# Performance work log

Measured on AMD Instinct MI355X. Metric: run time of the kernel, lower is better.

Reference implementation:

```python
import jax, jax.numpy as jnp
import numpy as np

B, N1, N2, D, H = 16, 1024, 1024, 1024, 16
DH = D // H  # head dim = 64
NEG = jnp.float32(-1e30)  # mask fill value (avoids -inf NaNs, bf16-safe)


def setup_inputs() -> dict:
    key = jax.random.key(0)
    ks = jax.random.split(key, 8)
    s = 0.02
    q = jax.random.normal(ks[0], (B, N1, D), dtype=jnp.float32)
    x = jax.random.normal(ks[1], (B, N2, D), dtype=jnp.float32)
    Wq = jax.random.normal(ks[2], (D, D), dtype=jnp.float32) * s
    Wk = jax.random.normal(ks[3], (D, D), dtype=jnp.float32) * s
    Wv = jax.random.normal(ks[4], (D, D), dtype=jnp.float32) * s
    Wo = jax.random.normal(ks[5], (D, D), dtype=jnp.float32) * s
    bq = jnp.zeros((D,), jnp.float32)
    bk = jnp.zeros((D,), jnp.float32)
    bv = jnp.zeros((D,), jnp.float32)
    bo = jnp.zeros((D,), jnp.float32)
    adj_mat = jax.random.randint(ks[6], (N1, N2), 0, 2).astype(jnp.bool_)
    return {"q": q, "x": x, "Wq": Wq, "bq": bq, "Wk": Wk, "bk": bk,
            "Wv": Wv, "bv": bv, "Wo": Wo, "bo": bo, "adj_mat": adj_mat}


def reference(q, x, Wq, bq, Wk, bk, Wv, bv, Wo, bo, adj_mat):
    b = q.shape[0]
    # QKV projections (torch Linear: y = x @ W.T + b), split into heads
    qh = (q @ Wq.T + bq).reshape(b, N1, H, DH).transpose(0, 2, 1, 3)  # [B,H,N1,DH]
    kh = (x @ Wk.T + bk).reshape(b, N2, H, DH).transpose(0, 2, 1, 3)  # [B,H,N2,DH]
    vh = (x @ Wv.T + bv).reshape(b, N2, H, DH).transpose(0, 2, 1, 3)  # [B,H,N2,DH]
    # masked SDPA with fixed adjacency mask (broadcast over batch & heads)
    scale = jnp.asarray(DH, qh.dtype) ** -0.5
    scores = jnp.einsum("bhqd,bhkd->bhqk", qh, kh) * scale           # [B,H,N1,N2]
    scores = jnp.where(adj_mat, scores, NEG)
    attn = jax.nn.softmax(scores, axis=-1)
    o = jnp.einsum("bhqk,bhkd->bhqd", attn, vh)                      # [B,H,N1,DH]
    o = o.transpose(0, 2, 1, 3).reshape(b, N1, D)
    return o @ Wo.T + bo
```

## Files before the change

### kernel.cpp

```cpp
#include <hip/hip_runtime.h>


typedef float f32x4 __attribute__((ext_vector_type(4)));
typedef float f32x16 __attribute__((ext_vector_type(16)));
typedef __bf16 bf16x8 __attribute__((ext_vector_type(8)));

#define QSCALE 0.18033688f

__device__ __forceinline__ unsigned short f2bf(float f) {
    unsigned u = __builtin_bit_cast(unsigned, f);
    unsigned r = u + 0x7fffu + ((u >> 16) & 1u);
    return (unsigned short)(r >> 16);
}
__device__ __forceinline__ unsigned pk2(float a, float b) {
    return (unsigned)f2bf(a) | ((unsigned)f2bf(b) << 16);
}

__global__ __launch_bounds__(256) void cvt_bf16(const float* __restrict__ s0,
                                                unsigned short* __restrict__ d0,
                                                const float* __restrict__ s1,
                                                unsigned short* __restrict__ d1) {
    const float* src = blockIdx.y ? s1 : s0;
    unsigned short* dst = blockIdx.y ? d1 : d0;
    const int idx = blockIdx.x * 256 + threadIdx.x;
    float4 a = ((const float4*)src)[idx * 2];
    float4 b = ((const float4*)src)[idx * 2 + 1];
    uint4 u;
    u.x = pk2(a.x, a.y); u.y = pk2(a.z, a.w);
    u.z = pk2(b.x, b.y); u.w = pk2(b.z, b.w);
    ((uint4*)dst)[idx] = u;
}

__global__ __launch_bounds__(256) void cvt_w4(const float* __restrict__ W0,
                                              const float* __restrict__ W1,
                                              const float* __restrict__ W2,
                                              const float* __restrict__ W3,
                                              unsigned short* __restrict__ o0,
                                              unsigned short* __restrict__ o1,
                                              unsigned short* __restrict__ o2,
                                              unsigned short* __restrict__ o3) {
    const float* s = (blockIdx.y == 0) ? W0 : (blockIdx.y == 1) ? W1
                   : (blockIdx.y == 2) ? W2 : W3;
    unsigned short* d = (blockIdx.y == 0) ? o0 : (blockIdx.y == 1) ? o1
                      : (blockIdx.y == 2) ? o2 : o3;
    const int idx = blockIdx.x * 256 + threadIdx.x;
    float4 a = ((const float4*)s)[idx * 2];
    float4 b = ((const float4*)s)[idx * 2 + 1];
    uint4 u;
    u.x = pk2(a.x, a.y); u.y = pk2(a.z, a.w);
    u.z = pk2(b.x, b.y); u.w = pk2(b.z, b.w);
    ((uint4*)d)[idx] = u;
}

template <int OUTM>
__global__ __launch_bounds__(256, 2) void gemm2(const unsigned short* __restrict__ A,
                                                const unsigned short* __restrict__ W,
                                                const float* __restrict__ bias,
                                                void* __restrict__ Cp,
                                                float scale) {
    constexpr int N = 1024, K = 1024;
    __shared__ unsigned short As[2][128 * 64];
    __shared__ unsigned short Bs[2][128 * 64];

    const int t    = threadIdx.x;
    const int wave = t >> 6;
    const int lane = t & 63;
    const int bid  = blockIdx.x;
    const int xcd  = bid & 7;
    const int jj   = bid >> 3;
    const int n0   = (jj & 7) * 128;
    const int m0   = (xcd * 16 + (jj >> 3)) * 128;
    const int wr   = (wave >> 1) * 64;
    const int wc   = (wave & 1) * 64;
    const int lm   = lane & 15;
    const int quad = lane >> 4;

    int aoff[4], boff[4];
#pragma unroll
    for (int i = 0; i < 4; i++) {
        const int slot = wave * 256 + i * 64 + lane;
        const int r = slot >> 3;
        const int csrc = (slot & 7) ^ (r & 7);
        aoff[i] = (m0 + r) * K + csrc * 8;
        boff[i] = (n0 + r) * K + csrc * 8;
    }

    auto STAGE = [&](int cb, int k0) {
#pragma unroll
        for (int i = 0; i < 4; i++) {
            __builtin_amdgcn_global_load_lds(
                (const __attribute__((address_space(1))) unsigned int*)(A + aoff[i] + k0),
                (__attribute__((address_space(3))) unsigned int*)((char*)&As[cb][0] + wave * 4096 + i * 1024),
                16, 0, 0);
            __builtin_amdgcn_global_load_lds(
                (const __attribute__((address_space(1))) unsigned int*)(W + boff[i] + k0),
                (__attribute__((address_space(3))) unsigned int*)((char*)&Bs[cb][0] + wave * 4096 + i * 1024),
                16, 0, 0);
        }
    };

    f32x4 acc[4][4] = {};

    STAGE(0, 0);
    __syncthreads();

    int cur = 0;
    for (int k0 = 0; k0 < K; k0 += 64) {
        if (k0 + 64 < K) STAGE(cur ^ 1, k0 + 64);

        bf16x8 af[2][4], bfr[2][4];
#pragma unroll
        for (int ks = 0; ks < 2; ks++)
#pragma unroll
            for (int i = 0; i < 4; i++) {
                const int pos = ((ks * 4 + quad) ^ (lm & 7)) * 16;
                af[ks][i]  = *(const bf16x8*)((const char*)&As[cur][0] + (wr + i * 16 + lm) * 128 + pos);
                bfr[ks][i] = *(const bf16x8*)((const char*)&Bs[cur][0] + (wc + i * 16 + lm) * 128 + pos);
            }
#pragma unroll
        for (int ks = 0; ks < 2; ks++)
#pragma unroll
            for (int i = 0; i < 4; i++)
#pragma unroll
                for (int j = 0; j < 4; j++)
                    acc[i][j] = __builtin_amdgcn_mfma_f32_16x16x32_bf16(af[ks][i], bfr[ks][j],
                                                                        acc[i][j], 0, 0, 0);
        __syncthreads();
        cur ^= 1;
    }

#pragma unroll
    for (int i = 0; i < 4; i++) {
        const int row = m0 + wr + i * 16 + quad * 4;
#pragma unroll
        for (int j = 0; j < 4; j++) {
            const int col = n0 + wc + j * 16 + lm;
            const float bb = bias[col];
            if constexpr (OUTM == 2) {
                const int bi = row >> 10, n2 = row & 1023;
                const int hh = col >> 6, dh = col & 63;
                uint2 pkd;
                pkd.x = pk2((acc[i][j][0] + bb) * scale, (acc[i][j][1] + bb) * scale);
                pkd.y = pk2((acc[i][j][2] + bb) * scale, (acc[i][j][3] + bb) * scale);
                *(uint2*)&((unsigned short*)Cp)[((size_t)((bi * 16 + hh) * 64 + dh) << 10) + n2] = pkd;
            } else {
#pragma unroll
                for (int rr = 0; rr < 4; rr++) {
                    const float v = (acc[i][j][rr] + bb) * scale;
                    if constexpr (OUTM == 0)
                        ((unsigned short*)Cp)[(size_t)(row + rr) * N + col] = f2bf(v);
                    else
                        ((float*)Cp)[(size_t)(row + rr) * N + col] = v;
                }
            }
        }
    }
}

template <bool A_BF16, int OUTM>
__global__ __launch_bounds__(256) void gemm_bt(const void* __restrict__ Ap,
                                               const float* __restrict__ Wp,
                                               const float* __restrict__ bias,
                                               void* __restrict__ Cp,
                                               float scale) {
    constexpr int N = 1024, K = 1024;
    __shared__ unsigned short As[128 * 40];
    __shared__ unsigned short Bs[128 * 40];

    const int t    = threadIdx.x;
    const int n0   = blockIdx.x * 128;
    const int m0   = blockIdx.y * 128;
    const int wave = t >> 6;
    const int lane = t & 63;
    const int wr   = (wave >> 1) * 64;
    const int wc   = (wave & 1) * 64;
    const int lm   = lane & 15;
    const int quad = lane >> 4;
    const int kfr  = quad * 8;
    const int srow  = t >> 1;
    const int shalf = (t & 1) * 16;

    f32x4 acc[4][4] = {};

    for (int k0 = 0; k0 < K; k0 += 32) {
        {
            unsigned short* dst = &As[srow * 40 + shalf];
            if constexpr (A_BF16) {
                const unsigned short* pa =
                    (const unsigned short*)Ap + (size_t)(m0 + srow) * K + k0 + shalf;
                *(uint4*)dst       = *(const uint4*)pa;
                *(uint4*)(dst + 8) = *(const uint4*)(pa + 8);
            } else {
                const float* pa = (const float*)Ap + (size_t)(m0 + srow) * K + k0 + shalf;
                float4 f0 = *(const float4*)(pa + 0);
                float4 f1 = *(const float4*)(pa + 4);
                float4 f2 = *(const float4*)(pa + 8);
                float4 f3 = *(const float4*)(pa + 12);
                uint4 u0, u1;
                u0.x = pk2(f0.x, f0.y); u0.y = pk2(f0.z, f0.w);
                u0.z = pk2(f1.x, f1.y); u0.w = pk2(f1.z, f1.w);
                u1.x = pk2(f2.x, f2.y); u1.y = pk2(f2.z, f2.w);
                u1.z = pk2(f3.x, f3.y); u1.w = pk2(f3.z, f3.w);
                *(uint4*)dst       = u0;
                *(uint4*)(dst + 8) = u1;
            }
        }
        {
            const float* pb = Wp + (size_t)(n0 + srow) * K + k0 + shalf;
            float4 f0 = *(const float4*)(pb + 0);
            float4 f1 = *(const float4*)(pb + 4);
            float4 f2 = *(const float4*)(pb + 8);
            float4 f3 = *(const float4*)(pb + 12);
            uint4 u0, u1;
            u0.x = pk2(f0.x, f0.y); u0.y = pk2(f0.z, f0.w);
            u0.z = pk2(f1.x, f1.y); u0.w = pk2(f1.z, f1.w);
            u1.x = pk2(f2.x, f2.y); u1.y = pk2(f2.z, f2.w);
            u1.z = pk2(f3.x, f3.y); u1.w = pk2(f3.z, f3.w);
            unsigned short* dst = &Bs[srow * 40 + shalf];
            *(uint4*)dst       = u0;
            *(uint4*)(dst + 8) = u1;
        }
        __syncthreads();

        bf16x8 af[4], bfr[4];
#pragma unroll
        for (int i = 0; i < 4; i++)
            af[i] = *reinterpret_cast<const bf16x8*>(&As[(wr + i * 16 + lm) * 40 + kfr]);
#pragma unroll
        for (int j = 0; j < 4; j++)
            bfr[j] = *reinterpret_cast<const bf16x8*>(&Bs[(wc + j * 16 + lm) * 40 + kfr]);
#pragma unroll
        for (int i = 0; i < 4; i++)
#pragma unroll
            for (int j = 0; j < 4; j++)
                acc[i][j] = __builtin_amdgcn_mfma_f32_16x16x32_bf16(af[i], bfr[j],
                                                                    acc[i][j], 0, 0, 0);
        __syncthreads();
    }

#pragma unroll
    for (int i = 0; i < 4; i++) {
        const int row = m0 + wr + i * 16 + quad * 4;
#pragma unroll
        for (int j = 0; j < 4; j++) {
            const int col = n0 + wc + j * 16 + lm;
            const float bb = bias[col];
#pragma unroll
            for (int rr = 0; rr < 4; rr++) {
                const float v = (acc[i][j][rr] + bb) * scale;
                const int m = row + rr;
                if constexpr (OUTM == 0) {
                    ((unsigned short*)Cp)[(size_t)m * N + col] = f2bf(v);
                } else if constexpr (OUTM == 1) {
                    ((float*)Cp)[(size_t)m * N + col] = v;
                } else {
                    const int bi = m >> 10, n2 = m & 1023;
                    const int hh = col >> 6, dh = col & 63;
                    ((unsigned short*)Cp)[((size_t)((bi * 16 + hh) * 64 + dh) << 10) + n2] =
                        f2bf(v);
                }
            }
        }
    }
}

__global__ __launch_bounds__(256) void pack_adj(const int* __restrict__ adj,
                                                unsigned* __restrict__ adjm) {
    const int idx = blockIdx.x * 256 + threadIdx.x;
    const int* src = adj + (size_t)idx * 32;
    unsigned w = 0;
#pragma unroll
    for (int i = 0; i < 32; i++) w |= (src[i] != 0 ? 1u : 0u) << i;
    adjm[idx] = w;
}

__global__ __launch_bounds__(256, 3) void attn_kernel(const unsigned short* __restrict__ Q,
                                                      const unsigned short* __restrict__ K,
                                                      const unsigned short* __restrict__ Vt,
                                                      const unsigned* __restrict__ adjm,
                                                      unsigned short* __restrict__ O) {
    __shared__ unsigned short Kbuf[2][4112];
    __shared__ unsigned short Vbuf[2][4112];

    const int t    = threadIdx.x;
    const int wave = t >> 6;
    const int lane = t & 63;
    const int l32  = lane & 31;
    const int hi   = lane >> 5;

    const int bid   = blockIdx.x;
    const int xcd   = bid & 7;
    const int jj    = bid >> 3;
    const int group = xcd * 32 + (jj >> 3);
    const int q0    = (jj & 7) * 128;
    const int h     = group & 15;
    const int b     = group >> 4;

    const int qrow = q0 + wave * 32 + l32;

    int    ldofs[2];
    size_t kofs[2], vofs[2];
#pragma unroll
    for (int i = 0; i < 2; i++) {
        const int slot = i * 256 + t;
        const int r    = slot >> 3;
        const int cs   = (slot & 7) ^ (r & 7);
        ldofs[i] = slot * 16;
        kofs[i]  = (size_t)(b * 1024 + r) * 1024 + h * 64 + cs * 8;
        vofs[i]  = ((size_t)((b * 16 + h) * 64 + r) << 10) + cs * 8;
    }

    bf16x8 aq[4];
    {
        const unsigned short* qp =
            Q + ((size_t)(b * 1024 + qrow) * 1024 + h * 64 + hi * 8);
#pragma unroll
        for (int s = 0; s < 4; s++)
            aq[s] = __builtin_bit_cast(bf16x8, *(const uint4*)(qp + s * 16));
    }

    bf16x8 bones;
    {
        uint4 u; u.x = 0x3F803F80u; u.y = u.x; u.z = u.x; u.w = u.x;
        bones = __builtin_bit_cast(bf16x8, u);
    }

    f32x16 of0 = {}, of1 = {}, ol = {};

    auto STAGE = [&](int bi, int c) {
        const size_t j0 = (size_t)c * 64;
#pragma unroll
        for (int i = 0; i < 2; i++) {
            __builtin_amdgcn_global_load_lds(
                (const __attribute__((address_space(1))) unsigned int*)(K + kofs[i] + j0 * 1024),
                (__attribute__((address_space(3))) unsigned int*)((char*)&Kbuf[bi][0] + ldofs[i]),
                16, 0, 0);
            __builtin_amdgcn_global_load_lds(
                (const __attribute__((address_space(1))) unsigned int*)(Vt + vofs[i] + j0),
                (__attribute__((address_space(3))) unsigned int*)((char*)&Vbuf[bi][0] + ldofs[i]),
                16, 0, 0);
        }
    };

    STAGE(0, 0);
    __syncthreads();

    int bi = 0;
    for (int c = 0; c < 16; ++c) {
        const uint2 mw = *(const uint2*)&adjm[(size_t)qrow * 32 + c * 2];

        if (c < 15) STAGE(bi ^ 1, c + 1);

        f32x16 sf[2] = {{}, {}};
        __builtin_amdgcn_s_setprio(1);
#pragma unroll
        for (int f = 0; f < 2; f++)
#pragma unroll
            for (int s = 0; s < 4; s++) {
                const int pos = ((2 * s + hi) ^ (l32 & 7)) * 16;
                const bf16x8 kf =
                    *(const bf16x8*)((const char*)&Kbuf[bi][0] + (f * 32 + l32) * 128 + pos);
                sf[f] = __builtin_amdgcn_mfma_f32_32x32x16_bf16(kf, aq[s], sf[f], 0, 0, 0);
            }
        __builtin_amdgcn_s_setprio(0);

        unsigned d[2][4][2];
#pragma unroll
        for (int f = 0; f < 2; f++) {
            const unsigned wh = ((f == 0) ? mw.x : mw.y) >> (hi * 4);
            float p[16];
#pragma unroll
            for (int r = 0; r < 16; r++) {
                const unsigned bit = (wh >> ((r & 3) + 8 * (r >> 2))) & 1u;
                p[r] = __builtin_amdgcn_exp2f(bit ? sf[f][r] : -1e30f);
            }
#pragma unroll
            for (int a = 0; a < 4; a++)
#pragma unroll
                for (int bb = 0; bb < 2; bb++) {
                    unsigned dd;
                    asm("v_cvt_pk_bf16_f32 %0, %1, %2"
                        : "=v"(dd) : "v"(p[4 * a + 2 * bb]), "v"(p[4 * a + 2 * bb + 1]));
                    d[f][a][bb] = dd;
                }
        }

        bf16x8 tA[4];
#pragma unroll
        for (int s = 0; s < 4; s++) {
            const int f = s >> 1, sg = s & 1;
            unsigned A0 = d[f][2 * sg][0], B0 = d[f][2 * sg + 1][0];
            unsigned A1 = d[f][2 * sg][1], B1 = d[f][2 * sg + 1][1];
            asm("v_permlane32_swap_b32 %0, %1" : "+v"(A0), "+v"(B0));
            asm("v_permlane32_swap_b32 %0, %1" : "+v"(A1), "+v"(B1));
            uint4 td; td.x = A0; td.y = A1; td.z = B0; td.w = B1;
            tA[s] = __builtin_bit_cast(bf16x8, td);
        }

        __builtin_amdgcn_s_setprio(1);
#pragma unroll
        for (int s = 0; s < 4; s++) {
            const int pos = ((2 * s + hi) ^ (l32 & 7)) * 16;
            const bf16x8 v0 = *(const bf16x8*)((const char*)&Vbuf[bi][0] + l32 * 128 + pos);
            const bf16x8 v1 = *(const bf16x8*)((const char*)&Vbuf[bi][0] + (32 + l32) * 128 + pos);
            of0 = __builtin_amdgcn_mfma_f32_32x32x16_bf16(tA[s], v0, of0, 0, 0, 0);
            of1 = __builtin_amdgcn_mfma_f32_32x32x16_bf16(tA[s], v1, of1, 0, 0, 0);
            ol  = __builtin_amdgcn_mfma_f32_32x32x16_bf16(tA[s], bones, ol, 0, 0, 0);
        }
        __builtin_amdgcn_s_setprio(0);

        __syncthreads();
        bi ^= 1;
    }

#pragma unroll
    for (int r = 0; r < 16; r++) {
        const float iv = 1.0f / ol[r];
        const size_t row = (size_t)(b * 1024 + q0 + wave * 32 +
                                    (r & 3) + 8 * (r >> 2) + 4 * hi);
        unsigned short* op = O + row * 1024 + h * 64 + l32;
        op[0]  = f2bf(of0[r] * iv);
        op[32] = f2bf(of1[r] * iv);
    }
}

extern "C" void kernel_launch(void* const* d_in, const int* in_sizes, int n_in,
                              void* d_out, int out_size, void* d_ws, size_t ws_size,
                              hipStream_t stream) {
    const float* q  = (const float*)d_in[0];
    const float* x  = (const float*)d_in[1];
    const float* Wq = (const float*)d_in[2];
    const float* bq = (const float*)d_in[3];
    const float* Wk = (const float*)d_in[4];
    const float* bk = (const float*)d_in[5];
    const float* Wv = (const float*)d_in[6];
    const float* bv = (const float*)d_in[7];
    const float* Wo = (const float*)d_in[8];
    const float* bo = (const float*)d_in[9];
    const int* adj  = (const int*)d_in[10];
    float* out = (float*)d_out;

    const size_t MB = 1024 * 1024;
    char* w = (char*)d_ws;

    dim3 gswz(1024), tb(256);
    const size_t FULL_WS = 168 * MB + 128 * 1024;

    if (ws_size >= FULL_WS) {
        unsigned short* qb  = (unsigned short*)(w);
        unsigned short* xb  = (unsigned short*)(w + 32 * MB);
        unsigned short* Wqb = (unsigned short*)(w + 64 * MB);
        unsigned short* Wkb = (unsigned short*)(w + 66 * MB);
        unsigned short* Wvb = (unsigned short*)(w + 68 * MB);
        unsigned short* Wob = (unsigned short*)(w + 70 * MB);
        unsigned short* Qb  = (unsigned short*)(w + 72 * MB);
        unsigned short* Kb  = (unsigned short*)(w + 104 * MB);
        unsigned short* Vtb = (unsigned short*)(w + 136 * MB);
        unsigned* adjm      = (unsigned*)(w + 168 * MB);
        unsigned short* Ob  = qb;

        hipLaunchKernelGGL(cvt_bf16, dim3(8192, 2), tb, 0, stream, q, qb, x, xb);
        hipLaunchKernelGGL(cvt_w4, dim3(512, 4), tb, 0, stream, Wq, Wk, Wv, Wo,
                           Wqb, Wkb, Wvb, Wob);
        hipLaunchKernelGGL(pack_adj, dim3(128), tb, 0, stream, adj, adjm);

        hipLaunchKernelGGL((gemm2<0>), gswz, tb, 0, stream, qb, Wqb, bq, (void*)Qb, QSCALE);
        hipLaunchKernelGGL((gemm2<0>), gswz, tb, 0, stream, xb, Wkb, bk, (void*)Kb, 1.0f);
        hipLaunchKernelGGL((gemm2<2>), gswz, tb, 0, stream, xb, Wvb, bv, (void*)Vtb, 1.0f);
        hipLaunchKernelGGL(attn_kernel, dim3(2048), tb, 0, stream, Qb, Kb, Vtb, adjm, Ob);
        hipLaunchKernelGGL((gemm2<1>), gswz, tb, 0, stream, Ob, Wob, bo, (void*)out, 1.0f);
    } else {
        unsigned short* Qb  = (unsigned short*)(w);
        unsigned short* Kb  = (unsigned short*)(w + 32 * MB);
        unsigned short* Vtb = (unsigned short*)(w + 64 * MB);
        unsigned short* Ob  = (unsigned short*)(w + 96 * MB);
        unsigned* adjm      = (unsigned*)(w + 128 * MB);

        hipLaunchKernelGGL(pack_adj, dim3(128), tb, 0, stream, adj, adjm);
        hipLaunchKernelGGL((gemm_bt<false, 0>), dim3(8, 128), tb, 0, stream,
                           (const void*)q, Wq, bq, (void*)Qb, QSCALE);
        hipLaunchKernelGGL((gemm_bt<false, 0>), dim3(8, 128), tb, 0, stream,
                           (const void*)x, Wk, bk, (void*)Kb, 1.0f);
        hipLaunchKernelGGL((gemm_bt<false, 2>), dim3(8, 128), tb, 0, stream,
                           (const void*)x, Wv, bv, (void*)Vtb, 1.0f);
        hipLaunchKernelGGL(attn_kernel, dim3(2048), tb, 0, stream, Qb, Kb, Vtb, adjm, Ob);
        hipLaunchKernelGGL((gemm_bt<true, 1>), dim3(8, 128), tb, 0, stream,
                           (const void*)Ob, Wo, bo, (void*)out, 1.0f);
    }
}
```

Baseline: 448.9 us.

## Enlarge projection GEMM tiles to 256x256 with 512-thread blocks and finer waits

Replaces the 128x128 bf16 GEMM with a 256x256 tile kernel using 8 waves, each computing a 128x64 sub-tile, which halves global traffic per FLOP and raises MFMA work per LDS load. The K-loop now uses explicit vmcnt waits with raw s_barrier instead of __syncthreads, and raises wave priority around MFMA bursts. The grid drops to 256 blocks, so with 256 CUs there is about one block per CU and no tail, at the cost of more registers and 128KB LDS per block. Attention LDS padding is also removed.

```diff
diff --git a/kernel.cpp b/kernel.cpp
--- a/kernel.cpp
+++ b/kernel.cpp
@@ -53,36 +53,52 @@
 }
 
 template <int OUTM>
-__global__ __launch_bounds__(256, 2) void gemm2(const unsigned short* __restrict__ A,
-                                                const unsigned short* __restrict__ W,
-                                                const float* __restrict__ bias,
-                                                void* __restrict__ Cp,
-                                                float scale) {
+__global__ __launch_bounds__(512, 2) void gemm256(const unsigned short* __restrict__ A,
+                                                  const unsigned short* __restrict__ W,
+                                                  const float* __restrict__ bias,
+                                                  void* __restrict__ Cp,
+                                                  float scale) {
     constexpr int N = 1024, K = 1024;
-    __shared__ unsigned short As[2][128 * 64];
-    __shared__ unsigned short Bs[2][128 * 64];
+    __shared__ unsigned short As[2][256 * 64];
+    __shared__ unsigned short Bs[2][256 * 64];
 
     const int t    = threadIdx.x;
     const int wave = t >> 6;
     const int lane = t & 63;
-    const int bid  = blockIdx.x;
-    const int xcd  = bid & 7;
-    const int jj   = bid >> 3;
-    const int n0   = (jj & 7) * 128;
-    const int m0   = (xcd * 16 + (jj >> 3)) * 128;
-    const int wr   = (wave >> 1) * 64;
-    const int wc   = (wave & 1) * 64;
     const int lm   = lane & 15;
     const int quad = lane >> 4;
 
-    int aoff[4], boff[4];
+    const int bid = blockIdx.x;
+    const int xcd = bid & 7;
+    const int jj  = bid >> 3;
+    const int n0  = (xcd & 3) * 256;
+    const int m0  = ((xcd >> 2) * 32 + jj) * 256;
+
+    const int wr = (wave >> 2) * 128;
+    const int wc = (wave & 3) * 64;
+
+    const int rh = wave >> 2;
+    const int wl = wave & 3;
+    const int bh = (wave >> 1) & 1;
+    const int bl = (wave & 1) | ((wave >> 2) << 1);
+
+    int aoff[4], aldo[4], boff[4], bldo[4];
 #pragma unroll
     for (int i = 0; i < 4; i++) {
-        const int slot = wave * 256 + i * 64 + lane;
-        const int r = slot >> 3;
-        const int csrc = (slot & 7) ^ (r & 7);
-        aoff[i] = (m0 + r) * K + csrc * 8;
-        boff[i] = (n0 + r) * K + csrc * 8;
+        {
+            const int slot = (wl * 4 + i) * 64 + lane;
+            const int r    = slot >> 3;
+            const int csrc = (slot & 7) ^ (r & 7);
+            aoff[i] = (m0 + rh * 128 + r) * K + csrc * 8;
+            aldo[i] = rh * 16384 + slot * 16;
+        }
+        {
+            const int slot = (bl * 4 + i) * 64 + lane;
+            const int r    = slot >> 3;
+            const int csrc = (slot & 7) ^ (r & 7);
+            boff[i] = (n0 + bh * 128 + r) * K + csrc * 8;
+            bldo[i] = bh * 16384 + slot * 16;
+        }
     }
 
     auto STAGE = [&](int cb, int k0) {
@@ -90,47 +106,69 @@
         for (int i = 0; i < 4; i++) {
             __builtin_amdgcn_global_load_lds(
                 (const __attribute__((address_space(1))) unsigned int*)(A + aoff[i] + k0),
-                (__attribute__((address_space(3))) unsigned int*)((char*)&As[cb][0] + wave * 4096 + i * 1024),
+                (__attribute__((address_space(3))) unsigned int*)((char*)&As[cb][0] + aldo[i]),
                 16, 0, 0);
             __builtin_amdgcn_global_load_lds(
                 (const __attribute__((address_space(1))) unsigned int*)(W + boff[i] + k0),
-                (__attribute__((address_space(3))) unsigned int*)((char*)&Bs[cb][0] + wave * 4096 + i * 1024),
+                (__attribute__((address_space(3))) unsigned int*)((char*)&Bs[cb][0] + bldo[i]),
                 16, 0, 0);
         }
     };
 
-    f32x4 acc[4][4] = {};
+    f32x4 acc[8][4] = {};
 
     STAGE(0, 0);
-    __syncthreads();
 
     int cur = 0;
-    for (int k0 = 0; k0 < K; k0 += 64) {
-        if (k0 + 64 < K) STAGE(cur ^ 1, k0 + 64);
-
-        bf16x8 af[2][4], bfr[2][4];
-#pragma unroll
-        for (int ks = 0; ks < 2; ks++)
-#pragma unroll
-            for (int i = 0; i < 4; i++) {
-                const int pos = ((ks * 4 + quad) ^ (lm & 7)) * 16;
-                af[ks][i]  = *(const bf16x8*)((const char*)&As[cur][0] + (wr + i * 16 + lm) * 128 + pos);
-                bfr[ks][i] = *(const bf16x8*)((const char*)&Bs[cur][0] + (wc + i * 16 + lm) * 128 + pos);
+    for (int kt = 0; kt < 16; ++kt) {
+        if (kt < 15) {
+            STAGE(cur ^ 1, (kt + 1) * 64);
+            asm volatile("s_waitcnt vmcnt(8)" ::: "memory");
+        } else {
+            asm volatile("s_waitcnt vmcnt(0)" ::: "memory");
+        }
+        __builtin_amdgcn_s_barrier();
+        __builtin_amdgcn_sched_barrier(0);
+
+        bf16x8 bfr[4][2];
+#pragma unroll
+        for (int j = 0; j < 4; j++)
+#pragma unroll
+            for (int ks = 0; ks < 2; ks++) {
+                const int row = wc + j * 16 + lm;
+                const int pos = ((ks * 4 + quad) ^ (row & 7)) * 16;
+                bfr[j][ks] = *(const bf16x8*)((const char*)&Bs[cur][0] + row * 128 + pos);
             }
 #pragma unroll
-        for (int ks = 0; ks < 2; ks++)
-#pragma unroll
-            for (int i = 0; i < 4; i++)
-#pragma unroll
-                for (int j = 0; j < 4; j++)
-                    acc[i][j] = __builtin_amdgcn_mfma_f32_16x16x32_bf16(af[ks][i], bfr[ks][j],
-                                                                        acc[i][j], 0, 0, 0);
-        __syncthreads();
+        for (int ih = 0; ih < 2; ih++) {
+            bf16x8 af[4][2];
+#pragma unroll
+            for (int i4 = 0; i4 < 4; i4++)
+#pragma unroll
+                for (int ks = 0; ks < 2; ks++) {
+                    const int row = wr + ih * 64 + i4 * 16 + lm;
+                    const int pos = ((ks * 4 + quad) ^ (row & 7)) * 16;
+                    af[i4][ks] = *(const bf16x8*)((const char*)&As[cur][0] + row * 128 + pos);
+                }
+            __builtin_amdgcn_s_setprio(1);
+#pragma unroll
+            for (int ks = 0; ks < 2; ks++)
+#pragma unroll
+                for (int i4 = 0; i4 < 4; i4++)
+#pragma unroll
+                    for (int j = 0; j < 4; j++)
+                        acc[ih * 4 + i4][j] = __builtin_amdgcn_mfma_f32_16x16x32_bf16(
+                            af[i4][ks], bfr[j][ks], acc[ih * 4 + i4][j], 0, 0, 0);
+            __builtin_amdgcn_s_setprio(0);
+        }
+
+        asm volatile("s_waitcnt lgkmcnt(0)" ::: "memory");
+        __builtin_amdgcn_s_barrier();
         cur ^= 1;
     }
 
 #pragma unroll
-    for (int i = 0; i < 4; i++) {
+    for (int i = 0; i < 8; i++) {
         const int row = m0 + wr + i * 16 + quad * 4;
 #pragma unroll
         for (int j = 0; j < 4; j++) {
@@ -279,8 +317,8 @@
                                                       const unsigned short* __restrict__ Vt,
                                                       const unsigned* __restrict__ adjm,
                                                       unsigned short* __restrict__ O) {
-    __shared__ unsigned short Kbuf[2][4112];
-    __shared__ unsigned short Vbuf[2][4112];
+    __shared__ unsigned short Kbuf[2][4096];
+    __shared__ unsigned short Vbuf[2][4096];
 
     const int t    = threadIdx.x;
     const int wave = t >> 6;
@@ -443,7 +481,7 @@
     const size_t MB = 1024 * 1024;
     char* w = (char*)d_ws;
 
-    dim3 gswz(1024), tb(256);
+    dim3 g256(256), tb(256), tb512(512);
     const size_t FULL_WS = 168 * MB + 128 * 1024;
 
     if (ws_size >= FULL_WS) {
@@ -464,11 +502,11 @@
                            Wqb, Wkb, Wvb, Wob);
         hipLaunchKernelGGL(pack_adj, dim3(128), tb, 0, stream, adj, adjm);
 
-        hipLaunchKernelGGL((gemm2<0>), gswz, tb, 0, stream, qb, Wqb, bq, (void*)Qb, QSCALE);
-        hipLaunchKernelGGL((gemm2<0>), gswz, tb, 0, stream, xb, Wkb, bk, (void*)Kb, 1.0f);
-        hipLaunchKernelGGL((gemm2<2>), gswz, tb, 0, stream, xb, Wvb, bv, (void*)Vtb, 1.0f);
+        hipLaunchKernelGGL((gemm256<0>), g256, tb512, 0, stream, qb, Wqb, bq, (void*)Qb, QSCALE);
+        hipLaunchKernelGGL((gemm256<0>), g256, tb512, 0, stream, xb, Wkb, bk, (void*)Kb, 1.0f);
+        hipLaunchKernelGGL((gemm256<2>), g256, tb512, 0, stream, xb, Wvb, bv, (void*)Vtb, 1.0f);
         hipLaunchKernelGGL(attn_kernel, dim3(2048), tb, 0, stream, Qb, Kb, Vtb, adjm, Ob);
-        hipLaunchKernelGGL((gemm2<1>), gswz, tb, 0, stream, Ob, Wob, bo, (void*)out, 1.0f);
+        hipLaunchKernelGGL((gemm256<1>), g256, tb512, 0, stream, Ob, Wob, bo, (void*)out, 1.0f);
     } else {
         unsigned short* Qb  = (unsigned short*)(w);
         unsigned short* Kb  = (unsigned short*)(w + 32 * MB);
```

Result: no change. 452.2 us (+0.7%).

## Merge Q/K/V projection GEMMs into one launch, add MFMA priority, shrink attention LDS

Applied to the files above, without the earlier changes.

Runs the three projection GEMMs as a single 3072-block launch whose block index selects input, weight, bias and output layout, so the three kernels no longer serialize with a tail between each. It also raises wave priority around the MFMA loop with s_setprio, and removes the padding from the attention kernel's K/V shared buffers. The output mode is now a runtime branch inside the merged kernel, and dropping the LDS padding may bring back bank conflicts.

```diff
diff --git a/kernel.cpp b/kernel.cpp
--- a/kernel.cpp
+++ b/kernel.cpp
@@ -52,12 +52,12 @@
     ((uint4*)d)[idx] = u;
 }
 
-template <int OUTM>
-__global__ __launch_bounds__(256, 2) void gemm2(const unsigned short* __restrict__ A,
-                                                const unsigned short* __restrict__ W,
-                                                const float* __restrict__ bias,
-                                                void* __restrict__ Cp,
-                                                float scale) {
+template <int OUTM_CONST>
+__device__ __forceinline__ void gemm_body(const unsigned short* __restrict__ A,
+                                          const unsigned short* __restrict__ W,
+                                          const float* __restrict__ bias,
+                                          void* __restrict__ Cp,
+                                          float scale, int b2, int outm_rt) {
     constexpr int N = 1024, K = 1024;
     __shared__ unsigned short As[2][128 * 64];
     __shared__ unsigned short Bs[2][128 * 64];
@@ -65,9 +65,8 @@
     const int t    = threadIdx.x;
     const int wave = t >> 6;
     const int lane = t & 63;
-    const int bid  = blockIdx.x;
-    const int xcd  = bid & 7;
-    const int jj   = bid >> 3;
+    const int xcd  = b2 & 7;
+    const int jj   = b2 >> 3;
     const int n0   = (jj & 7) * 128;
     const int m0   = (xcd * 16 + (jj >> 3)) * 128;
     const int wr   = (wave >> 1) * 64;
@@ -117,6 +116,7 @@
                 af[ks][i]  = *(const bf16x8*)((const char*)&As[cur][0] + (wr + i * 16 + lm) * 128 + pos);
                 bfr[ks][i] = *(const bf16x8*)((const char*)&Bs[cur][0] + (wc + i * 16 + lm) * 128 + pos);
             }
+        __builtin_amdgcn_s_setprio(1);
 #pragma unroll
         for (int ks = 0; ks < 2; ks++)
 #pragma unroll
@@ -125,9 +125,12 @@
                 for (int j = 0; j < 4; j++)
                     acc[i][j] = __builtin_amdgcn_mfma_f32_16x16x32_bf16(af[ks][i], bfr[ks][j],
                                                                         acc[i][j], 0, 0, 0);
+        __builtin_amdgcn_s_setprio(0);
         __syncthreads();
         cur ^= 1;
     }
+
+    const int outm = (OUTM_CONST >= 0) ? OUTM_CONST : outm_rt;
 
 #pragma unroll
     for (int i = 0; i < 4; i++) {
@@ -136,25 +139,56 @@
         for (int j = 0; j < 4; j++) {
             const int col = n0 + wc + j * 16 + lm;
             const float bb = bias[col];
-            if constexpr (OUTM == 2) {
+            if (outm == 2) {
                 const int bi = row >> 10, n2 = row & 1023;
                 const int hh = col >> 6, dh = col & 63;
                 uint2 pkd;
                 pkd.x = pk2((acc[i][j][0] + bb) * scale, (acc[i][j][1] + bb) * scale);
                 pkd.y = pk2((acc[i][j][2] + bb) * scale, (acc[i][j][3] + bb) * scale);
                 *(uint2*)&((unsigned short*)Cp)[((size_t)((bi * 16 + hh) * 64 + dh) << 10) + n2] = pkd;
+            } else if (outm == 0) {
+#pragma unroll
+                for (int rr = 0; rr < 4; rr++)
+                    ((unsigned short*)Cp)[(size_t)(row + rr) * N + col] =
+                        f2bf((acc[i][j][rr] + bb) * scale);
             } else {
 #pragma unroll
-                for (int rr = 0; rr < 4; rr++) {
-                    const float v = (acc[i][j][rr] + bb) * scale;
-                    if constexpr (OUTM == 0)
-                        ((unsigned short*)Cp)[(size_t)(row + rr) * N + col] = f2bf(v);
-                    else
-                        ((float*)Cp)[(size_t)(row + rr) * N + col] = v;
-                }
+                for (int rr = 0; rr < 4; rr++)
+                    ((float*)Cp)[(size_t)(row + rr) * N + col] = (acc[i][j][rr] + bb) * scale;
             }
         }
     }
+}
+
+__global__ __launch_bounds__(256, 2) void gemm_qkv(const unsigned short* __restrict__ qb,
+                                                   const unsigned short* __restrict__ xb,
+                                                   const unsigned short* __restrict__ Wqb,
+                                                   const unsigned short* __restrict__ Wkb,
+                                                   const unsigned short* __restrict__ Wvb,
+                                                   const float* __restrict__ bq,
+                                                   const float* __restrict__ bk,
+                                                   const float* __restrict__ bv,
+                                                   unsigned short* __restrict__ Qo,
+                                                   unsigned short* __restrict__ Ko,
+                                                   unsigned short* __restrict__ Vo) {
+    const int bid = blockIdx.x;
+    const int z   = bid >> 10;
+    const int b2  = bid & 1023;
+    const unsigned short* A = (z == 0) ? qb : xb;
+    const unsigned short* W = (z == 0) ? Wqb : (z == 1) ? Wkb : Wvb;
+    const float* bias       = (z == 0) ? bq : (z == 1) ? bk : bv;
+    void* Cp                = (z == 0) ? (void*)Qo : (z == 1) ? (void*)Ko : (void*)Vo;
+    const float scale       = (z == 0) ? QSCALE : 1.0f;
+    gemm_body<-1>(A, W, bias, Cp, scale, b2, (z == 2) ? 2 : 0);
+}
+
+template <int OUTM>
+__global__ __launch_bounds__(256, 2) void gemm2(const unsigned short* __restrict__ A,
+                                                const unsigned short* __restrict__ W,
+                                                const float* __restrict__ bias,
+                                                void* __restrict__ Cp,
+                                                float scale) {
+    gemm_body<OUTM>(A, W, bias, Cp, scale, blockIdx.x, OUTM);
 }
 
 template <bool A_BF16, int OUTM>
@@ -279,8 +313,8 @@
                                                       const unsigned short* __restrict__ Vt,
                                                       const unsigned* __restrict__ adjm,
                                                       unsigned short* __restrict__ O) {
-    __shared__ unsigned short Kbuf[2][4112];
-    __shared__ unsigned short Vbuf[2][4112];
+    __shared__ unsigned short Kbuf[2][4096];
+    __shared__ unsigned short Vbuf[2][4096];
 
     const int t    = threadIdx.x;
     const int wave = t >> 6;
@@ -443,7 +477,7 @@
     const size_t MB = 1024 * 1024;
     char* w = (char*)d_ws;
 
-    dim3 gswz(1024), tb(256);
+    dim3 tb(256);
     const size_t FULL_WS = 168 * MB + 128 * 1024;
 
     if (ws_size >= FULL_WS) {
@@ -464,11 +498,10 @@
                            Wqb, Wkb, Wvb, Wob);
         hipLaunchKernelGGL(pack_adj, dim3(128), tb, 0, stream, adj, adjm);
 
-        hipLaunchKernelGGL((gemm2<0>), gswz, tb, 0, stream, qb, Wqb, bq, (void*)Qb, QSCALE);
-        hipLaunchKernelGGL((gemm2<0>), gswz, tb, 0, stream, xb, Wkb, bk, (void*)Kb, 1.0f);
-        hipLaunchKernelGGL((gemm2<2>), gswz, tb, 0, stream, xb, Wvb, bv, (void*)Vtb, 1.0f);
+        hipLaunchKernelGGL(gemm_qkv, dim3(3072), tb, 0, stream,
+                           qb, xb, Wqb, Wkb, Wvb, bq, bk, bv, Qb, Kb, Vtb);
         hipLaunchKernelGGL(attn_kernel, dim3(2048), tb, 0, stream, Qb, Kb, Vtb, adjm, Ob);
-        hipLaunchKernelGGL((gemm2<1>), gswz, tb, 0, stream, Ob, Wob, bo, (void*)out, 1.0f);
+        hipLaunchKernelGGL((gemm2<1>), dim3(1024), tb, 0, stream, Ob, Wob, bo, (void*)out, 1.0f);
     } else {
         unsigned short* Qb  = (unsigned short*)(w);
         unsigned short* Kb  = (unsigned short*)(w + 32 * MB);
```

Result: no change. 449.7 us (+0.2%).
